# Kernel optimization log

Measured on AMD Instinct MI355X. Metric: run time of the kernel, lower is better.

## Reference

```python
import jax, jax.numpy as jnp
import numpy as np

NUM_USERS = 100000
NUM_ITEMS = 50000
HIDDEN = 64
NUM_LAYERS = 3
NUM_EDGES = 1200000
N = NUM_USERS + NUM_ITEMS


def setup_inputs() -> dict:
    key = jax.random.key(0)
    k_e, k_u, k_i, k_w, k_b = jax.random.split(key, 5)
    edge_index = jax.random.randint(k_e, (2, NUM_EDGES), 0, N, dtype=jnp.int32)
    users_emb = jax.random.normal(k_u, (NUM_USERS, HIDDEN), dtype=jnp.float32) * 0.01
    items_emb = jax.random.normal(k_i, (NUM_ITEMS, HIDDEN), dtype=jnp.float32) * 0.01
    # GCNConv linear weights (glorot-ish) and zero biases, stacked over layers
    scale = 1.0 / np.sqrt(HIDDEN)
    Ws = jax.random.uniform(k_w, (NUM_LAYERS, HIDDEN, HIDDEN), dtype=jnp.float32,
                            minval=-scale, maxval=scale)
    bs = jnp.zeros((NUM_LAYERS, HIDDEN), dtype=jnp.float32)
    return {"edge_index": edge_index, "users_emb": users_emb,
            "items_emb": items_emb, "Ws": Ws, "bs": bs}


def reference(edge_index, users_emb, items_emb, Ws, bs):
    # GraphSAGEModel.forward: concat user/item embeddings, run num_layers GCNConv
    # (PyG defaults: add self-loops, symmetric D^-1/2 A D^-1/2 normalization, bias).
    x = jnp.concatenate([users_emb, items_emb], axis=0)  # [N, H]

    self_loops = jnp.arange(N, dtype=edge_index.dtype)
    src = jnp.concatenate([edge_index[0], self_loops])  # [E+N]
    dst = jnp.concatenate([edge_index[1], self_loops])

    ones = jnp.ones(src.shape[0], dtype=x.dtype)
    deg = jax.ops.segment_sum(ones, dst, num_segments=N)  # in-degree incl self loop
    dinv = jnp.where(deg > 0, jax.lax.rsqrt(deg), 0.0)
    norm = dinv[src] * dinv[dst]  # [E+N], graph-constant across layers

    for l in range(NUM_LAYERS):
        h = x @ Ws[l]                       # linear transform [N, H]
        msg = h[src] * norm[:, None]        # gather + scale
        x = jax.ops.segment_sum(msg, dst, num_segments=N) + bs[l]
    return (x[:NUM_USERS], users_emb, x[NUM_USERS:], items_emb)
```

## Files before the change

### kernel.cpp

```cpp
#include <hip/hip_runtime.h>
#include <hip/hip_fp16.h>

#define NU 100000
#define NI 50000
#define NN 150000
#define HH 64
#define NE 1200000

#define SCAN_CHUNK 1024
#define NBLK ((NN + SCAN_CHUNK - 1) / SCAN_CHUNK)
#define AGG_BLOCKS (NN / 8)
#define UBLK ((NN + 255) / 256)

__global__ __launch_bounds__(256) void k_rank(const int4* __restrict__ dst4,
                                              int* __restrict__ counts,
                                              int4* __restrict__ rank4,
                                              __half* __restrict__ pad0,
                                              __half* __restrict__ pad1) {
    if (blockIdx.x == 0 && threadIdx.x < 16) {
        if (threadIdx.x < 8) ((int4*)pad0)[threadIdx.x] = make_int4(0, 0, 0, 0);
        else                 ((int4*)pad1)[threadIdx.x - 8] = make_int4(0, 0, 0, 0);
    }
    int t = blockIdx.x * blockDim.x + threadIdx.x;
    if (t >= NE / 8) return;
    int4 d0 = dst4[2 * t], d1 = dst4[2 * t + 1];
    int4 r0, r1;
    r0.x = atomicAdd(&counts[d0.x], 1);
    r0.y = atomicAdd(&counts[d0.y], 1);
    r0.z = atomicAdd(&counts[d0.z], 1);
    r0.w = atomicAdd(&counts[d0.w], 1);
    r1.x = atomicAdd(&counts[d1.x], 1);
    r1.y = atomicAdd(&counts[d1.y], 1);
    r1.z = atomicAdd(&counts[d1.z], 1);
    r1.w = atomicAdd(&counts[d1.w], 1);
    rank4[2 * t]     = r0;
    rank4[2 * t + 1] = r1;
}

__global__ __launch_bounds__(256) void k_scan(const int* __restrict__ counts,
                                              float* __restrict__ dinv,
                                              float* __restrict__ dinv2,
                                              int* __restrict__ row_ptr,
                                              unsigned int* __restrict__ state) {
    __shared__ int sd[256];
    __shared__ int s_prefix;
    int t = threadIdx.x;
    int b = blockIdx.x;
    int base = b * SCAN_CHUNK + t * 4;
    int c[4];
    if (base + 3 < NN) {
        int4 v = *(const int4*)(counts + base);
        c[0] = v.x; c[1] = v.y; c[2] = v.z; c[3] = v.w;
    } else {
#pragma unroll
        for (int i = 0; i < 4; ++i) c[i] = (base + i < NN) ? counts[base + i] : 0;
    }
#pragma unroll
    for (int i = 0; i < 4; ++i)
        if (base + i < NN) {
            dinv[base + i]  = rsqrtf((float)(c[i] + 1));
            dinv2[base + i] = 1.0f / (float)(c[i] + 1);
        }

    int tt = c[0] + c[1] + c[2] + c[3];
    sd[t] = tt; __syncthreads();
    for (int off = 1; off < 256; off <<= 1) {
        int x = (t >= off) ? sd[t - off] : 0;
        __syncthreads();
        sd[t] += x;
        __syncthreads();
    }

    if (t == 0) {
        unsigned int agg = (unsigned int)sd[255];
        if (b == 0) {
            __hip_atomic_store(&state[0], (2u << 30) | agg, __ATOMIC_RELEASE,
                               __HIP_MEMORY_SCOPE_AGENT);
            s_prefix = 0;
        } else {
            __hip_atomic_store(&state[b], (1u << 30) | agg, __ATOMIC_RELEASE,
                               __HIP_MEMORY_SCOPE_AGENT);
            unsigned int prefix = 0;
            int p = b - 1;
            while (true) {
                unsigned int s = __hip_atomic_load(&state[p], __ATOMIC_ACQUIRE,
                                                   __HIP_MEMORY_SCOPE_AGENT);
                unsigned int fl = s >> 30;
                if (fl == 0u) { __builtin_amdgcn_s_sleep(1); continue; }
                prefix += s & 0x3FFFFFFFu;
                if (fl == 2u) break;
                --p;
            }
            __hip_atomic_store(&state[b], (2u << 30) | (prefix + agg),
                               __ATOMIC_RELEASE, __HIP_MEMORY_SCOPE_AGENT);
            s_prefix = (int)prefix;
        }
    }
    __syncthreads();

    int off0 = s_prefix + (sd[t] - tt);
    int run = 0;
#pragma unroll
    for (int i = 0; i < 4; ++i) {
        if (base + i < NN) row_ptr[base + i] = off0 + run;
        run += c[i];
    }
    if (b == NBLK - 1 && t == 0) row_ptr[NN] = NE;
}

#define CONCAT_BLOCKS (NN * (HH / 4) / 256)
#define FILL_BLOCKS   ((NE / 8 + 255) / 256)

__global__ __launch_bounds__(256) void k_concat_fill(
    const float4* __restrict__ users, const float4* __restrict__ items,
    const float* __restrict__ dinv, __half2* __restrict__ xs, float4* __restrict__ out,
    const int4* __restrict__ src4, const int4* __restrict__ dst4,
    const int4* __restrict__ rank4, const int* __restrict__ row_ptr,
    int* __restrict__ col) {
    if (blockIdx.x < CONCAT_BLOCKS) {
        int i = blockIdx.x * 256 + threadIdx.x;
        const int UB = NU * (HH / 4);
        float4 v;
        if (i < UB) {
            v = users[i];
            out[UB + i] = v;
        } else {
            int j = i - UB;
            v = items[j];
            out[2 * UB + NI * (HH / 4) + j] = v;
        }
        float dv = dinv[i >> 4];
        xs[2 * i]     = __halves2half2(__float2half_rn(v.x * dv), __float2half_rn(v.y * dv));
        xs[2 * i + 1] = __halves2half2(__float2half_rn(v.z * dv), __float2half_rn(v.w * dv));
    } else {
        int t = (blockIdx.x - CONCAT_BLOCKS) * 256 + threadIdx.x;
        if (t >= NE / 8) return;
        int4 s0 = src4[2 * t],  s1 = src4[2 * t + 1];
        int4 d0 = dst4[2 * t],  d1 = dst4[2 * t + 1];
        int4 r0 = rank4[2 * t], r1 = rank4[2 * t + 1];
        int p0 = row_ptr[d0.x], p1 = row_ptr[d0.y], p2 = row_ptr[d0.z], p3 = row_ptr[d0.w];
        int p4 = row_ptr[d1.x], p5 = row_ptr[d1.y], p6 = row_ptr[d1.z], p7 = row_ptr[d1.w];
        col[p0 + r0.x] = s0.x;
        col[p1 + r0.y] = s0.y;
        col[p2 + r0.z] = s0.z;
        col[p3 + r0.w] = s0.w;
        col[p4 + r1.x] = s1.x;
        col[p5 + r1.y] = s1.y;
        col[p6 + r1.z] = s1.z;
        col[p7 + r1.w] = s1.w;
    }
}

template <int MODE>
__global__ __launch_bounds__(256) void k_aggregate(
    const __half* __restrict__ x, __half* __restrict__ y,
    const float* __restrict__ scale,
    const int* __restrict__ row_ptr, const int* __restrict__ col,
    const float* __restrict__ dinv, const float* __restrict__ pin,
    float* __restrict__ uout, float* __restrict__ pout,
    const float* __restrict__ Wfull, const float* __restrict__ bfull,
    float* __restrict__ What, float* __restrict__ cvec) {
    int bid = blockIdx.x;
    if (MODE != 0) {
        const int EXTRA = (MODE == 1) ? (UBLK + 1) : UBLK;
        if (bid < EXTRA) {
            if (MODE == 1 && bid == UBLK) {
                __shared__ float W12[HH * HH];
                int t = threadIdx.x;
                int r = t >> 2, j0 = (t & 3) * 16;
                const float* W0 = Wfull;
                const float* W1 = Wfull + HH * HH;
                const float* W2 = Wfull + 2 * HH * HH;
                float acc[16];
#pragma unroll
                for (int j = 0; j < 16; ++j) acc[j] = 0.f;
                for (int k = 0; k < HH; ++k) {
                    float a = W1[r * HH + k];
                    const float* bp = W2 + k * HH + j0;
#pragma unroll
                    for (int j = 0; j < 16; ++j) acc[j] += a * bp[j];
                }
#pragma unroll
                for (int j = 0; j < 16; ++j) W12[r * HH + j0 + j] = acc[j];
                if (t < HH) {
                    float s = 0.f;
                    for (int k = 0; k < HH; ++k) s += bfull[HH + k] * W2[k * HH + t];
                    cvec[HH + t] = s;
                }
                __syncthreads();
#pragma unroll
                for (int j = 0; j < 16; ++j) acc[j] = 0.f;
                for (int k = 0; k < HH; ++k) {
                    float a = W0[r * HH + k];
                    const float* bp = W12 + k * HH + j0;
#pragma unroll
                    for (int j = 0; j < 16; ++j) acc[j] += a * bp[j];
                }
#pragma unroll
                for (int j = 0; j < 16; ++j) What[r * HH + j0 + j] = acc[j];
                if (t < HH) {
                    float s = 0.f;
                    for (int k = 0; k < HH; ++k) s += bfull[k] * W12[k * HH + t];
                    cvec[t] = s;
                }
                return;
            }
            int n = bid * 256 + threadIdx.x;
            if (n < NN) {
                float dv = dinv[n];
                float acc = pin[n];
                int e1 = row_ptr[n + 1];
                for (int e = row_ptr[n]; e < e1; ++e) acc += pin[col[e]];
                float u = dv * acc;
                uout[n] = u;
                if (MODE == 1) pout[n] = dv * u;
            }
            return;
        }
        bid -= EXTRA;
    }

    int lane = threadIdx.x & 63;
    int wave = bid * 4 + (threadIdx.x >> 6);
    int na = wave * 2;
    if (na >= NN) return;
    int nb = na + 1;
    int q  = lane >> 4;
    int f4 = (lane & 15) << 2;

    float a0 = 0.f, a1 = 0.f, a2 = 0.f, a3 = 0.f;
    float b0 = 0.f, b1 = 0.f, b2 = 0.f, b3 = 0.f;

#define GATHER(r, c0, c1, c2, c3)                                          \
    {                                                                      \
        uint2 raw = *(const uint2*)(x + (size_t)(r) * HH + f4);            \
        float2 f0 = __half22float2(*(__half2*)&raw.x);                     \
        float2 f1 = __half22float2(*(__half2*)&raw.y);                     \
        c0 += f0.x; c1 += f0.y; c2 += f1.x; c3 += f1.y;                    \
    }

    int ea = row_ptr[na], enda = row_ptr[na + 1];
    int eb = enda,        endb = row_ptr[nb + 1];

    {
        int ia = ea + q - 1;
        int ib = eb + q - 1;
        int rA = (q == 0) ? na : ((ia < enda) ? col[ia] : NN);
        int rB = (q == 0) ? nb : ((ib < endb) ? col[ib] : NN);
        GATHER(rA, a0, a1, a2, a3);
        GATHER(rB, b0, b1, b2, b3);
        ea += 3; eb += 3;
    }
    while (ea < enda || eb < endb) {
        int iA1 = ea + q,     iA2 = ea + 4 + q;
        int iB1 = eb + q,     iB2 = eb + 4 + q;
        int rA1 = (iA1 < enda) ? col[iA1] : NN;
        int rA2 = (iA2 < enda) ? col[iA2] : NN;
        int rB1 = (iB1 < endb) ? col[iB1] : NN;
        int rB2 = (iB2 < endb) ? col[iB2] : NN;
        GATHER(rA1, a0, a1, a2, a3);
        GATHER(rA2, a0, a1, a2, a3);
        GATHER(rB1, b0, b1, b2, b3);
        GATHER(rB2, b0, b1, b2, b3);
        ea += 8; eb += 8;
    }
#undef GATHER

    a0 += __shfl_xor(a0, 16); a1 += __shfl_xor(a1, 16);
    a2 += __shfl_xor(a2, 16); a3 += __shfl_xor(a3, 16);
    b0 += __shfl_xor(b0, 16); b1 += __shfl_xor(b1, 16);
    b2 += __shfl_xor(b2, 16); b3 += __shfl_xor(b3, 16);
    a0 += __shfl_xor(a0, 32); a1 += __shfl_xor(a1, 32);
    a2 += __shfl_xor(a2, 32); a3 += __shfl_xor(a3, 32);
    b0 += __shfl_xor(b0, 32); b1 += __shfl_xor(b1, 32);
    b2 += __shfl_xor(b2, 32); b3 += __shfl_xor(b3, 32);

    if (lane < 32) {
        int   n  = (q == 0) ? na : nb;
        float dv = scale[n];
        float s0 = (q == 0) ? a0 : b0;
        float s1 = (q == 0) ? a1 : b1;
        float s2 = (q == 0) ? a2 : b2;
        float s3 = (q == 0) ? a3 : b3;
        __half2 h0 = __halves2half2(__float2half_rn(dv * s0), __float2half_rn(dv * s1));
        __half2 h1 = __halves2half2(__float2half_rn(dv * s2), __float2half_rn(dv * s3));
        uint2 packed;
        packed.x = *(unsigned int*)&h0;
        packed.y = *(unsigned int*)&h1;
        *(uint2*)(y + (size_t)n * HH + f4) = packed;
    }
}

#define GR 128
#define XSS 65
__global__ __launch_bounds__(256) void k_gemm_final(
    const __half* __restrict__ y, const float* __restrict__ W,
    const float* __restrict__ b2, const float* __restrict__ cvec,
    const float* __restrict__ u1, const float* __restrict__ u2,
    float* __restrict__ out_lo, float* __restrict__ out_hi) {
    __shared__ float xs[GR * XSS];
    __shared__ float ws[HH * HH];
    int t = threadIdx.x;
    int rowBase = blockIdx.x * GR;

    {
        const float4* W4 = (const float4*)W;
        float4* ws4 = (float4*)ws;
#pragma unroll
        for (int i = 0; i < 4; ++i) ws4[i * 256 + t] = W4[i * 256 + t];
    }
#pragma unroll
    for (int it = 0; it < 4; ++it) {
        int g = it * 256 + t;
        int r = g >> 3;
        int c0 = (g & 7) * 8;
        int row = rowBase + r;
        if (row < NN) {
            int4 raw = *(const int4*)(y + (size_t)row * HH + c0);
            __half2 h0 = *(__half2*)&raw.x, h1 = *(__half2*)&raw.y;
            __half2 h2 = *(__half2*)&raw.z, h3 = *(__half2*)&raw.w;
            float2 f0 = __half22float2(h0), f1 = __half22float2(h1);
            float2 f2 = __half22float2(h2), f3 = __half22float2(h3);
            float* dp = xs + r * XSS + c0;
            dp[0] = f0.x; dp[1] = f0.y; dp[2] = f1.x; dp[3] = f1.y;
            dp[4] = f2.x; dp[5] = f2.y; dp[6] = f3.x; dp[7] = f3.y;
        }
    }
    __syncthreads();

    int tx = t & 7;
    int ty = t >> 3;
    int j0 = tx * 8;
    int r0 = ty * 4;

    float acc[4][8];
#pragma unroll
    for (int i = 0; i < 4; ++i)
#pragma unroll
        for (int j = 0; j < 8; ++j) acc[i][j] = 0.f;

    for (int k = 0; k < HH; ++k) {
        float4 w0 = *(const float4*)(ws + k * HH + j0);
        float4 w1 = *(const float4*)(ws + k * HH + j0 + 4);
        float wv[8] = {w0.x, w0.y, w0.z, w0.w, w1.x, w1.y, w1.z, w1.w};
#pragma unroll
        for (int i = 0; i < 4; ++i) {
            float xv = xs[(r0 + i) * XSS + k];
#pragma unroll
            for (int j = 0; j < 8; ++j) acc[i][j] += xv * wv[j];
        }
    }

    float c0j[8], c1j[8], b2j[8];
#pragma unroll
    for (int j = 0; j < 8; ++j) {
        c0j[j] = cvec[j0 + j];
        c1j[j] = cvec[HH + j0 + j];
        b2j[j] = b2[j0 + j];
    }

#pragma unroll
    for (int i = 0; i < 4; ++i) {
        int r = rowBase + r0 + i;
        if (r >= NN) continue;
        float u2r = u2[r], u1r = u1[r];
        float base[8];
#pragma unroll
        for (int j = 0; j < 8; ++j) base[j] = u2r * c0j[j] + u1r * c1j[j] + b2j[j];
        float4 o0 = make_float4(acc[i][0] + base[0], acc[i][1] + base[1],
                                acc[i][2] + base[2], acc[i][3] + base[3]);
        float4 o1 = make_float4(acc[i][4] + base[4], acc[i][5] + base[5],
                                acc[i][6] + base[6], acc[i][7] + base[7]);
        float* d = (r < NU) ? (out_lo + (size_t)r * HH)
                            : (out_hi + (size_t)(r - NU) * HH);
        *(float4*)(d + j0) = o0;
        *(float4*)(d + j0 + 4) = o1;
    }
}

extern "C" void kernel_launch(void* const* d_in, const int* in_sizes, int n_in,
                              void* d_out, int out_size, void* d_ws, size_t ws_size,
                              hipStream_t stream) {
    const int*   edge  = (const int*)d_in[0];
    const int*   src   = edge;
    const int*   dst   = edge + NE;
    const float* users = (const float*)d_in[1];
    const float* items = (const float*)d_in[2];
    const float* Ws    = (const float*)d_in[3];
    const float* bs    = (const float*)d_in[4];
    float*       out   = (float*)d_out;

    char* w = (char*)d_ws;
    __half* Xs0     = (__half*)w; w += (size_t)(NN + 1) * HH * 2;
    __half* Xs1     = (__half*)w; w += (size_t)(NN + 1) * HH * 2;
    float*  dinv    = (float*)w;  w += (size_t)NN * 4;
    float*  dinv2   = (float*)w;  w += (size_t)NN * 4;
    float*  u1      = (float*)w;  w += (size_t)NN * 4;
    float*  p1u     = (float*)w;  w += (size_t)NN * 4;
    float*  u2      = (float*)w;  w += (size_t)NN * 4;
    float*  What    = (float*)w;  w += (size_t)HH * HH * 4;
    float*  cvec    = (float*)w;  w += (size_t)2 * HH * 4;
    unsigned int* state = (unsigned int*)w; w += 256 * 4;
    int*    counts  = (int*)w;    w += (size_t)NN * 4;
    int*    row_ptr = (int*)w;    w += (size_t)(NN + 1) * 4;
    w += 12;
    int*    col     = (int*)w;    w += (size_t)NE * 4;
    int*    rank    = (int*)w;    w += (size_t)NE * 4;
    (void)ws_size; (void)in_sizes; (void)n_in; (void)out_size;

    hipMemsetAsync(state, 0, (size_t)(256 + NN) * sizeof(int), stream);

    k_rank<<<(NE / 8 + 255) / 256, 256, 0, stream>>>(
        (const int4*)dst, counts, (int4*)rank,
        Xs0 + (size_t)NN * HH, Xs1 + (size_t)NN * HH);
    k_scan<<<NBLK, 256, 0, stream>>>(counts, dinv, dinv2, row_ptr, state);
    k_concat_fill<<<CONCAT_BLOCKS + FILL_BLOCKS, 256, 0, stream>>>(
        (const float4*)users, (const float4*)items, dinv, (__half2*)Xs0, (float4*)out,
        (const int4*)src, (const int4*)dst, (const int4*)rank, row_ptr, col);

    k_aggregate<1><<<UBLK + 1 + AGG_BLOCKS, 256, 0, stream>>>(
        Xs0, Xs1, dinv2, row_ptr, col, dinv, dinv, u1, p1u, Ws, bs, What, cvec);
    k_aggregate<2><<<UBLK + AGG_BLOCKS, 256, 0, stream>>>(
        Xs1, Xs0, dinv2, row_ptr, col, dinv, p1u, u2, nullptr, nullptr, nullptr,
        nullptr, nullptr);
    k_aggregate<0><<<AGG_BLOCKS, 256, 0, stream>>>(
        Xs0, Xs1, dinv, row_ptr, col, nullptr, nullptr, nullptr, nullptr, nullptr,
        nullptr, nullptr, nullptr);

    const int GEMM_BLOCKS = (NN + GR - 1) / GR;
    k_gemm_final<<<GEMM_BLOCKS, 256, 0, stream>>>(
        Xs1, What, bs + 2 * HH, cvec, u1, u2,
        out , out + (size_t)2 * NU * HH );
}
```

Measured before the change: 414.5 us.

## Fuse scalar bias-path aggregation into feature gather and widen gathers to 16 bytes

```diff
diff --git a/kernel.cpp b/kernel.cpp
--- a/kernel.cpp
+++ b/kernel.cpp
@@ -10,16 +10,19 @@
 #define SCAN_CHUNK 1024
 #define NBLK ((NN + SCAN_CHUNK - 1) / SCAN_CHUNK)
 #define AGG_BLOCKS (NN / 8)
-#define UBLK ((NN + 255) / 256)
 
 __global__ __launch_bounds__(256) void k_rank(const int4* __restrict__ dst4,
                                               int* __restrict__ counts,
                                               int4* __restrict__ rank4,
                                               __half* __restrict__ pad0,
-                                              __half* __restrict__ pad1) {
-    if (blockIdx.x == 0 && threadIdx.x < 16) {
-        if (threadIdx.x < 8) ((int4*)pad0)[threadIdx.x] = make_int4(0, 0, 0, 0);
-        else                 ((int4*)pad1)[threadIdx.x - 8] = make_int4(0, 0, 0, 0);
+                                              __half* __restrict__ pad1,
+                                              float* __restrict__ dinv,
+                                              float* __restrict__ p1u) {
+    if (blockIdx.x == 0 && threadIdx.x < 18) {
+        if (threadIdx.x < 8)       ((int4*)pad0)[threadIdx.x] = make_int4(0, 0, 0, 0);
+        else if (threadIdx.x < 16) ((int4*)pad1)[threadIdx.x - 8] = make_int4(0, 0, 0, 0);
+        else if (threadIdx.x == 16) dinv[NN] = 0.f;
+        else                        p1u[NN] = 0.f;
     }
     int t = blockIdx.x * blockDim.x + threadIdx.x;
     if (t >= NE / 8) return;
@@ -41,11 +44,57 @@
                                               float* __restrict__ dinv,
                                               float* __restrict__ dinv2,
                                               int* __restrict__ row_ptr,
-                                              unsigned int* __restrict__ state) {
-    __shared__ int sd[256];
+                                              unsigned int* __restrict__ state,
+                                              const float* __restrict__ Wfull,
+                                              const float* __restrict__ bfull,
+                                              float* __restrict__ What,
+                                              float* __restrict__ cvec) {
+    __shared__ float smem[HH * HH];
     __shared__ int s_prefix;
     int t = threadIdx.x;
     int b = blockIdx.x;
+
+    if (b == NBLK) {
+        int r = t >> 2, j0 = (t & 3) * 16;
+        const float* W0 = Wfull;
+        const float* W1 = Wfull + HH * HH;
+        const float* W2 = Wfull + 2 * HH * HH;
+        float acc[16];
+#pragma unroll
+        for (int j = 0; j < 16; ++j) acc[j] = 0.f;
+        for (int k = 0; k < HH; ++k) {
+            float a = W1[r * HH + k];
+            const float* bp = W2 + k * HH + j0;
+#pragma unroll
+            for (int j = 0; j < 16; ++j) acc[j] += a * bp[j];
+        }
+#pragma unroll
+        for (int j = 0; j < 16; ++j) smem[r * HH + j0 + j] = acc[j];
+        if (t < HH) {
+            float s = 0.f;
+            for (int k = 0; k < HH; ++k) s += bfull[HH + k] * W2[k * HH + t];
+            cvec[HH + t] = s;
+        }
+        __syncthreads();
+#pragma unroll
+        for (int j = 0; j < 16; ++j) acc[j] = 0.f;
+        for (int k = 0; k < HH; ++k) {
+            float a = W0[r * HH + k];
+            const float* bp = smem + k * HH + j0;
+#pragma unroll
+            for (int j = 0; j < 16; ++j) acc[j] += a * bp[j];
+        }
+#pragma unroll
+        for (int j = 0; j < 16; ++j) What[r * HH + j0 + j] = acc[j];
+        if (t < HH) {
+            float s = 0.f;
+            for (int k = 0; k < HH; ++k) s += bfull[k] * smem[k * HH + t];
+            cvec[t] = s;
+        }
+        return;
+    }
+
+    int* sd = (int*)smem;
     int base = b * SCAN_CHUNK + t * 4;
     int c[4];
     if (base + 3 < NN) {
@@ -108,30 +157,40 @@
     if (b == NBLK - 1 && t == 0) row_ptr[NN] = NE;
 }
 
-#define CONCAT_BLOCKS (NN * (HH / 4) / 256)
+#define CONCAT_BLOCKS ((NN * 8 + 255) / 256)
 #define FILL_BLOCKS   ((NE / 8 + 255) / 256)
 
 __global__ __launch_bounds__(256) void k_concat_fill(
     const float4* __restrict__ users, const float4* __restrict__ items,
-    const float* __restrict__ dinv, __half2* __restrict__ xs, float4* __restrict__ out,
+    const float* __restrict__ dinv, int4* __restrict__ xs4, float4* __restrict__ out,
     const int4* __restrict__ src4, const int4* __restrict__ dst4,
     const int4* __restrict__ rank4, const int* __restrict__ row_ptr,
     int* __restrict__ col) {
     if (blockIdx.x < CONCAT_BLOCKS) {
         int i = blockIdx.x * 256 + threadIdx.x;
-        const int UB = NU * (HH / 4);
-        float4 v;
-        if (i < UB) {
-            v = users[i];
-            out[UB + i] = v;
+        if (i >= NN * 8) return;
+        const int UB8 = NU * 8;
+        const int UB4 = NU * 16;
+        float4 v0, v1;
+        if (i < UB8) {
+            v0 = users[2 * i];
+            v1 = users[2 * i + 1];
+            out[UB4 + 2 * i]     = v0;
+            out[UB4 + 2 * i + 1] = v1;
         } else {
-            int j = i - UB;
-            v = items[j];
-            out[2 * UB + NI * (HH / 4) + j] = v;
-        }
-        float dv = dinv[i >> 4];
-        xs[2 * i]     = __halves2half2(__float2half_rn(v.x * dv), __float2half_rn(v.y * dv));
-        xs[2 * i + 1] = __halves2half2(__float2half_rn(v.z * dv), __float2half_rn(v.w * dv));
+            int j = i - UB8;
+            v0 = items[2 * j];
+            v1 = items[2 * j + 1];
+            out[2 * UB4 + NI * 16 + 2 * j]     = v0;
+            out[2 * UB4 + NI * 16 + 2 * j + 1] = v1;
+        }
+        float dv = dinv[i >> 3];
+        __half2 h[4];
+        h[0] = __halves2half2(__float2half_rn(v0.x * dv), __float2half_rn(v0.y * dv));
+        h[1] = __halves2half2(__float2half_rn(v0.z * dv), __float2half_rn(v0.w * dv));
+        h[2] = __halves2half2(__float2half_rn(v1.x * dv), __float2half_rn(v1.y * dv));
+        h[3] = __halves2half2(__float2half_rn(v1.z * dv), __float2half_rn(v1.w * dv));
+        xs4[i] = *(int4*)h;
     } else {
         int t = (blockIdx.x - CONCAT_BLOCKS) * 256 + threadIdx.x;
         if (t >= NE / 8) return;
@@ -151,143 +210,91 @@
     }
 }
 
-template <int MODE>
+template <int UMODE>
 __global__ __launch_bounds__(256) void k_aggregate(
     const __half* __restrict__ x, __half* __restrict__ y,
     const float* __restrict__ scale,
     const int* __restrict__ row_ptr, const int* __restrict__ col,
     const float* __restrict__ dinv, const float* __restrict__ pin,
-    float* __restrict__ uout, float* __restrict__ pout,
-    const float* __restrict__ Wfull, const float* __restrict__ bfull,
-    float* __restrict__ What, float* __restrict__ cvec) {
-    int bid = blockIdx.x;
-    if (MODE != 0) {
-        const int EXTRA = (MODE == 1) ? (UBLK + 1) : UBLK;
-        if (bid < EXTRA) {
-            if (MODE == 1 && bid == UBLK) {
-                __shared__ float W12[HH * HH];
-                int t = threadIdx.x;
-                int r = t >> 2, j0 = (t & 3) * 16;
-                const float* W0 = Wfull;
-                const float* W1 = Wfull + HH * HH;
-                const float* W2 = Wfull + 2 * HH * HH;
-                float acc[16];
-#pragma unroll
-                for (int j = 0; j < 16; ++j) acc[j] = 0.f;
-                for (int k = 0; k < HH; ++k) {
-                    float a = W1[r * HH + k];
-                    const float* bp = W2 + k * HH + j0;
-#pragma unroll
-                    for (int j = 0; j < 16; ++j) acc[j] += a * bp[j];
-                }
-#pragma unroll
-                for (int j = 0; j < 16; ++j) W12[r * HH + j0 + j] = acc[j];
-                if (t < HH) {
-                    float s = 0.f;
-                    for (int k = 0; k < HH; ++k) s += bfull[HH + k] * W2[k * HH + t];
-                    cvec[HH + t] = s;
-                }
-                __syncthreads();
-#pragma unroll
-                for (int j = 0; j < 16; ++j) acc[j] = 0.f;
-                for (int k = 0; k < HH; ++k) {
-                    float a = W0[r * HH + k];
-                    const float* bp = W12 + k * HH + j0;
-#pragma unroll
-                    for (int j = 0; j < 16; ++j) acc[j] += a * bp[j];
-                }
-#pragma unroll
-                for (int j = 0; j < 16; ++j) What[r * HH + j0 + j] = acc[j];
-                if (t < HH) {
-                    float s = 0.f;
-                    for (int k = 0; k < HH; ++k) s += bfull[k] * W12[k * HH + t];
-                    cvec[t] = s;
-                }
-                return;
-            }
-            int n = bid * 256 + threadIdx.x;
-            if (n < NN) {
-                float dv = dinv[n];
-                float acc = pin[n];
-                int e1 = row_ptr[n + 1];
-                for (int e = row_ptr[n]; e < e1; ++e) acc += pin[col[e]];
-                float u = dv * acc;
-                uout[n] = u;
-                if (MODE == 1) pout[n] = dv * u;
-            }
-            return;
-        }
-        bid -= EXTRA;
-    }
-
+    float* __restrict__ uout, float* __restrict__ pout) {
     int lane = threadIdx.x & 63;
-    int wave = bid * 4 + (threadIdx.x >> 6);
+    int wave = blockIdx.x * 4 + (threadIdx.x >> 6);
     int na = wave * 2;
     if (na >= NN) return;
     int nb = na + 1;
-    int q  = lane >> 4;
-    int f4 = (lane & 15) << 2;
-
-    float a0 = 0.f, a1 = 0.f, a2 = 0.f, a3 = 0.f;
-    float b0 = 0.f, b1 = 0.f, b2 = 0.f, b3 = 0.f;
-
-#define GATHER(r, c0, c1, c2, c3)                                          \
+    int o  = lane >> 3;
+    int f8 = (lane & 7) << 3;
+
+    float a[8], b[8];
+#pragma unroll
+    for (int j = 0; j < 8; ++j) { a[j] = 0.f; b[j] = 0.f; }
+    float ua = 0.f, ub = 0.f;
+
+#define GATHER(r, acc, uacc)                                               \
     {                                                                      \
-        uint2 raw = *(const uint2*)(x + (size_t)(r) * HH + f4);            \
-        float2 f0 = __half22float2(*(__half2*)&raw.x);                     \
-        float2 f1 = __half22float2(*(__half2*)&raw.y);                     \
-        c0 += f0.x; c1 += f0.y; c2 += f1.x; c3 += f1.y;                    \
+        int4 raw = *(const int4*)(x + (size_t)(r) * HH + f8);              \
+        if (UMODE) uacc += pin[r];                                         \
+        __half2* hp = (__half2*)&raw;                                      \
+        _Pragma("unroll")                                                  \
+        for (int j = 0; j < 4; ++j) {                                      \
+            float2 f = __half22float2(hp[j]);                              \
+            acc[2 * j] += f.x; acc[2 * j + 1] += f.y;                      \
+        }                                                                  \
     }
 
     int ea = row_ptr[na], enda = row_ptr[na + 1];
     int eb = enda,        endb = row_ptr[nb + 1];
 
     {
-        int ia = ea + q - 1;
-        int ib = eb + q - 1;
-        int rA = (q == 0) ? na : ((ia < enda) ? col[ia] : NN);
-        int rB = (q == 0) ? nb : ((ib < endb) ? col[ib] : NN);
-        GATHER(rA, a0, a1, a2, a3);
-        GATHER(rB, b0, b1, b2, b3);
-        ea += 3; eb += 3;
+        int ia = ea + o - 1;
+        int ib = eb + o - 1;
+        int rA = (o == 0) ? na : ((ia < enda) ? col[ia] : NN);
+        int rB = (o == 0) ? nb : ((ib < endb) ? col[ib] : NN);
+        GATHER(rA, a, ua);
+        GATHER(rB, b, ub);
+        ea += 7; eb += 7;
     }
     while (ea < enda || eb < endb) {
-        int iA1 = ea + q,     iA2 = ea + 4 + q;
-        int iB1 = eb + q,     iB2 = eb + 4 + q;
-        int rA1 = (iA1 < enda) ? col[iA1] : NN;
-        int rA2 = (iA2 < enda) ? col[iA2] : NN;
-        int rB1 = (iB1 < endb) ? col[iB1] : NN;
-        int rB2 = (iB2 < endb) ? col[iB2] : NN;
-        GATHER(rA1, a0, a1, a2, a3);
-        GATHER(rA2, a0, a1, a2, a3);
-        GATHER(rB1, b0, b1, b2, b3);
-        GATHER(rB2, b0, b1, b2, b3);
+        int iA = ea + o, iB = eb + o;
+        int rA = (iA < enda) ? col[iA] : NN;
+        int rB = (iB < endb) ? col[iB] : NN;
+        GATHER(rA, a, ua);
+        GATHER(rB, b, ub);
         ea += 8; eb += 8;
     }
 #undef GATHER
 
-    a0 += __shfl_xor(a0, 16); a1 += __shfl_xor(a1, 16);
-    a2 += __shfl_xor(a2, 16); a3 += __shfl_xor(a3, 16);
-    b0 += __shfl_xor(b0, 16); b1 += __shfl_xor(b1, 16);
-    b2 += __shfl_xor(b2, 16); b3 += __shfl_xor(b3, 16);
-    a0 += __shfl_xor(a0, 32); a1 += __shfl_xor(a1, 32);
-    a2 += __shfl_xor(a2, 32); a3 += __shfl_xor(a3, 32);
-    b0 += __shfl_xor(b0, 32); b1 += __shfl_xor(b1, 32);
-    b2 += __shfl_xor(b2, 32); b3 += __shfl_xor(b3, 32);
-
-    if (lane < 32) {
-        int   n  = (q == 0) ? na : nb;
+#pragma unroll
+    for (int j = 0; j < 8; ++j) {
+        a[j] += __shfl_xor(a[j], 8);  b[j] += __shfl_xor(b[j], 8);
+        a[j] += __shfl_xor(a[j], 16); b[j] += __shfl_xor(b[j], 16);
+        a[j] += __shfl_xor(a[j], 32); b[j] += __shfl_xor(b[j], 32);
+    }
+    if (UMODE) {
+        ua += __shfl_xor(ua, 8);  ub += __shfl_xor(ub, 8);
+        ua += __shfl_xor(ua, 16); ub += __shfl_xor(ub, 16);
+        ua += __shfl_xor(ua, 32); ub += __shfl_xor(ub, 32);
+    }
+
+    if (o < 2) {
+        int   n  = (o == 0) ? na : nb;
         float dv = scale[n];
-        float s0 = (q == 0) ? a0 : b0;
-        float s1 = (q == 0) ? a1 : b1;
-        float s2 = (q == 0) ? a2 : b2;
-        float s3 = (q == 0) ? a3 : b3;
-        __half2 h0 = __halves2half2(__float2half_rn(dv * s0), __float2half_rn(dv * s1));
-        __half2 h1 = __halves2half2(__float2half_rn(dv * s2), __float2half_rn(dv * s3));
-        uint2 packed;
-        packed.x = *(unsigned int*)&h0;
-        packed.y = *(unsigned int*)&h1;
-        *(uint2*)(y + (size_t)n * HH + f4) = packed;
+        __half2 h[4];
+#pragma unroll
+        for (int j = 0; j < 4; ++j) {
+            float x0 = (o == 0) ? a[2 * j]     : b[2 * j];
+            float x1 = (o == 0) ? a[2 * j + 1] : b[2 * j + 1];
+            h[j] = __halves2half2(__float2half_rn(dv * x0), __float2half_rn(dv * x1));
+        }
+        *(int4*)(y + (size_t)n * HH + f8) = *(int4*)h;
+    }
+    if (UMODE && lane < 2) {
+        int n = na + lane;
+        float s = ((lane == 0) ? ua : ub) * 0.125f;
+        float dvn = dinv[n];
+        float u = dvn * s;
+        uout[n] = u;
+        if (UMODE == 1) pout[n] = dvn * u;
     }
 }
 
@@ -393,10 +400,10 @@
     char* w = (char*)d_ws;
     __half* Xs0     = (__half*)w; w += (size_t)(NN + 1) * HH * 2;
     __half* Xs1     = (__half*)w; w += (size_t)(NN + 1) * HH * 2;
-    float*  dinv    = (float*)w;  w += (size_t)NN * 4;
+    float*  dinv    = (float*)w;  w += (size_t)(NN + 1) * 4;
     float*  dinv2   = (float*)w;  w += (size_t)NN * 4;
     float*  u1      = (float*)w;  w += (size_t)NN * 4;
-    float*  p1u     = (float*)w;  w += (size_t)NN * 4;
+    float*  p1u     = (float*)w;  w += (size_t)(NN + 1) * 4;
     float*  u2      = (float*)w;  w += (size_t)NN * 4;
     float*  What    = (float*)w;  w += (size_t)HH * HH * 4;
     float*  cvec    = (float*)w;  w += (size_t)2 * HH * 4;
@@ -412,20 +419,19 @@
 
     k_rank<<<(NE / 8 + 255) / 256, 256, 0, stream>>>(
         (const int4*)dst, counts, (int4*)rank,
-        Xs0 + (size_t)NN * HH, Xs1 + (size_t)NN * HH);
-    k_scan<<<NBLK, 256, 0, stream>>>(counts, dinv, dinv2, row_ptr, state);
+        Xs0 + (size_t)NN * HH, Xs1 + (size_t)NN * HH, dinv, p1u);
+    k_scan<<<NBLK + 1, 256, 0, stream>>>(counts, dinv, dinv2, row_ptr, state,
+                                         Ws, bs, What, cvec);
     k_concat_fill<<<CONCAT_BLOCKS + FILL_BLOCKS, 256, 0, stream>>>(
-        (const float4*)users, (const float4*)items, dinv, (__half2*)Xs0, (float4*)out,
+        (const float4*)users, (const float4*)items, dinv, (int4*)Xs0, (float4*)out,
         (const int4*)src, (const int4*)dst, (const int4*)rank, row_ptr, col);
 
-    k_aggregate<1><<<UBLK + 1 + AGG_BLOCKS, 256, 0, stream>>>(
-        Xs0, Xs1, dinv2, row_ptr, col, dinv, dinv, u1, p1u, Ws, bs, What, cvec);
-    k_aggregate<2><<<UBLK + AGG_BLOCKS, 256, 0, stream>>>(
-        Xs1, Xs0, dinv2, row_ptr, col, dinv, p1u, u2, nullptr, nullptr, nullptr,
-        nullptr, nullptr);
+    k_aggregate<1><<<AGG_BLOCKS, 256, 0, stream>>>(
+        Xs0, Xs1, dinv2, row_ptr, col, dinv, dinv, u1, p1u);
+    k_aggregate<2><<<AGG_BLOCKS, 256, 0, stream>>>(
+        Xs1, Xs0, dinv2, row_ptr, col, dinv, p1u, u2, nullptr);
     k_aggregate<0><<<AGG_BLOCKS, 256, 0, stream>>>(
-        Xs0, Xs1, dinv, row_ptr, col, nullptr, nullptr, nullptr, nullptr, nullptr,
-        nullptr, nullptr, nullptr);
+        Xs0, Xs1, dinv, row_ptr, col, nullptr, nullptr, nullptr, nullptr);
 
     const int GEMM_BLOCKS = (NN + GR - 1) / GR;
     k_gemm_final<<<GEMM_BLOCKS, 256, 0, stream>>>(
```

New measurement: 403.9 us. -2.6%, faster.
